# Performance work log

Hardware: AMD Instinct MI355X
Metric: run time of the kernel (lower is better)

Reference implementation:

```python
import jax, jax.numpy as jnp
import numpy as np

N = 16777216  # length of the returns series


def setup_inputs() -> dict:
    key = jax.random.key(0)
    returns = 0.01 * jax.random.normal(key, (N,), dtype=jnp.float32)
    return {
        "returns": returns,
        "omega": jnp.float32(0.01),
        "alpha": jnp.float32(0.1),
        "beta": jnp.float32(0.85),
    }


def reference(returns, omega, alpha, beta):
    # GARCH(1,1): h[0] = var(returns) (unbiased, matching torch.var default);
    # h[t] = omega + alpha * r[t-1]^2 + beta * h[t-1]
    h0 = jnp.var(returns, ddof=1)
    # drivers b_t = omega + alpha * r_{t-1}^2 for t = 1..n-1
    b = omega + alpha * jnp.square(returns[:-1])

    def step(h_prev, b_t):
        h_t = b_t + beta * h_prev
        return h_t, h_t

    _, h_rest = jax.lax.scan(step, h0, b)
    h = jnp.concatenate([h0[None], h_rest])  # [n]
    return jnp.sqrt(h), h
```

## Files before the change

kernel.cpp:

```cpp
#include <hip/hip_runtime.h>
#include <math.h>


#define KPW 2048
#define MAIN_BLOCK 256
#define FIX 256

typedef float v4f __attribute__((ext_vector_type(4)));

__global__ __launch_bounds__(MAIN_BLOCK, 8)
void garch_fused(const float* __restrict__ r, int n,
                 const float* __restrict__ pOmega, const float* __restrict__ pAlpha,
                 const float* __restrict__ pBeta,
                 float* __restrict__ out_sqrt, float* __restrict__ out_h,
                 double* __restrict__ partial) {
    const int lane = threadIdx.x & 63;
    const int wid  = threadIdx.x >> 6;
    const int gwave = (blockIdx.x * blockDim.x + threadIdx.x) >> 6;
    const int start = gwave * KPW;

    const float omega = *pOmega;
    const float alpha = *pAlpha;
    const float beta  = *pBeta;

    const float c1 = beta;
    const float c2 = c1 * c1;
    const float c4 = c2 * c2;
    const float c8 = c4 * c4;
    const float c16 = c8 * c8;
    const float c32 = c16 * c16;
    const float c64 = c32 * c32;
    const float c128 = c64 * c64;

    double acc_s = 0.0, acc_q = 0.0;

    if (start + KPW <= n) {
        float pw1 = 1.0f;
        { float p = c1; int e = lane;
          if (e & 1)  pw1 *= p; p *= p;
          if (e & 2)  pw1 *= p; p *= p;
          if (e & 4)  pw1 *= p; p *= p;
          if (e & 8)  pw1 *= p; p *= p;
          if (e & 16) pw1 *= p; p *= p;
          if (e & 32) pw1 *= p; }
        float pw32 = 1.0f;
        { float p = c32; int e = lane;
          if (e & 1)  pw32 *= p; p *= p;
          if (e & 2)  pw32 *= p; p *= p;
          if (e & 4)  pw32 *= p; p *= p;
          if (e & 8)  pw32 *= p; p *= p;
          if (e & 16) pw32 *= p; p *= p;
          if (e & 32) pw32 *= p; }

        const float4* r4p = (const float4*)r;
        const int base4 = (start >> 2) + lane * 8;

        float4 rv[8];
        #pragma unroll
        for (int k = 0; k < 8; ++k) rv[k] = r4p[base4 + k];

        float seed_ra = 0.0f, seed_rb = 0.0f, p0 = 0.0f;
        if (start > 0) {
            seed_ra = r[start - 2 - lane];
            seed_rb = r[start - 66 - lane];
            p0      = r[start - 1];
        }

        float h_prev = 0.0f;
        if (start > 0) {
            float ba = fmaf(alpha * seed_ra, seed_ra, omega);
            float bb = fmaf(alpha * seed_rb, seed_rb, omega);
            float part = pw1 * fmaf(c64, bb, ba);
            for (int d = 1; d < 64; d <<= 1) part += __shfl_xor(part, d, 64);
            h_prev = part;
        }

        #pragma unroll
        for (int k = 0; k < 8; k += 2) {
            float4 a = rv[k], b = rv[k + 1];
            float sf = ((a.x + a.y) + (a.z + a.w)) + ((b.x + b.y) + (b.z + b.w));
            float qf = fmaf(a.x, a.x, fmaf(a.y, a.y, fmaf(a.z, a.z, a.w * a.w)));
            qf = fmaf(b.x, b.x, fmaf(b.y, b.y, fmaf(b.z, b.z, fmaf(b.w, b.w, qf))));
            acc_s += (double)sf;
            acc_q += (double)qf;
        }

        float pprev = __shfl_up(rv[7].w, 1, 64);
        if (lane == 0) pprev = p0;

        float prev = pprev;
        float B = 0.0f;
        #pragma unroll
        for (int k = 0; k < 8; ++k) {
            float4 v = rv[k];
            float bb;
            bb = fmaf(alpha * prev, prev, omega);
            if (k == 0) { if (start == 0 && lane == 0) bb = 0.0f; B = bb; }
            else B = fmaf(c1, B, bb);
            prev = v.x;
            bb = fmaf(alpha * prev, prev, omega); B = fmaf(c1, B, bb); prev = v.y;
            bb = fmaf(alpha * prev, prev, omega); B = fmaf(c1, B, bb); prev = v.z;
            bb = fmaf(alpha * prev, prev, omega); B = fmaf(c1, B, bb); prev = v.w;
        }

        float t;
        t = __shfl_up(B, 1, 64); if (lane >= 1) B = fmaf(c32,  t, B);
        t = __shfl_up(B, 2, 64); if (lane >= 2) B = fmaf(c64,  t, B);
        t = __shfl_up(B, 4, 64); if (lane >= 4) B = fmaf(c128, t, B);

        float Bex = __shfl_up(B, 1, 64);
        if (lane == 0) Bex = 0.0f;
        float h = fmaf(pw32, h_prev, Bex);

        prev = pprev;
        #pragma unroll
        for (int k = 0; k < 8; ++k) {
            float4 v = rv[k];
            float bb;
            bb = fmaf(alpha * prev, prev, omega);
            if (k == 0 && start == 0 && lane == 0) bb = 0.0f;
            float h0v = fmaf(c1, h, bb);            prev = v.x;
            bb = fmaf(alpha * prev, prev, omega);
            float h1v = fmaf(c1, h0v, bb);          prev = v.y;
            bb = fmaf(alpha * prev, prev, omega);
            float h2v = fmaf(c1, h1v, bb);          prev = v.z;
            bb = fmaf(alpha * prev, prev, omega);
            float h3v = fmaf(c1, h2v, bb);          prev = v.w;
            h = h3v;

            v4f hs = {h0v, h1v, h2v, h3v};
            v4f sq = {sqrtf(h0v), sqrtf(h1v), sqrtf(h2v), sqrtf(h3v)};
            ((v4f*)out_h)[base4 + k]    = hs;
            ((v4f*)out_sqrt)[base4 + k] = sq;
        }
    } else if (start < n) {
        float h_prev = 0.0f;
        if (start > 0) {
            float pw1 = 1.0f;
            { float p = c1; int e = lane;
              if (e & 1)  pw1 *= p; p *= p;
              if (e & 2)  pw1 *= p; p *= p;
              if (e & 4)  pw1 *= p; p *= p;
              if (e & 8)  pw1 *= p; p *= p;
              if (e & 16) pw1 *= p; p *= p;
              if (e & 32) pw1 *= p; }
            float ra = r[start - 2 - lane];
            float rb = r[start - 66 - lane];
            float ba = fmaf(alpha * ra, ra, omega);
            float bb = fmaf(alpha * rb, rb, omega);
            float part = pw1 * fmaf(c64, bb, ba);
            for (int d = 1; d < 64; d <<= 1) part += __shfl_xor(part, d, 64);
            h_prev = part;
        }
        if (lane == 0) {
            float h = h_prev;
            float prevr = (start > 0) ? r[start - 1] : 0.0f;
            for (int tt = start; tt < n; ++tt) {
                float bb = fmaf(alpha * prevr, prevr, omega);
                if (tt == 0) bb = 0.0f;
                float hv = fmaf(beta, h, bb);
                out_sqrt[tt] = sqrtf(hv);
                out_h[tt] = hv;
                h = hv;
                prevr = r[tt];
                acc_s += (double)prevr;
                acc_q += (double)prevr * prevr;
            }
        }
    }

    for (int d = 1; d < 64; d <<= 1) {
        acc_s += __shfl_xor(acc_s, d, 64);
        acc_q += __shfl_xor(acc_q, d, 64);
    }
    __shared__ double ls[MAIN_BLOCK / 64], lq[MAIN_BLOCK / 64];
    if (lane == 0) { ls[wid] = acc_s; lq[wid] = acc_q; }
    __syncthreads();
    if (threadIdx.x == 0) {
        double S = 0.0, Q = 0.0;
        for (int w = 0; w < (int)(blockDim.x >> 6); ++w) { S += ls[w]; Q += lq[w]; }
        partial[2 * blockIdx.x]     = S;
        partial[2 * blockIdx.x + 1] = Q;
    }
}

__global__ void garch_finalize(const double* __restrict__ partial, int nblocks, int n,
                               const float* __restrict__ r,
                               const float* __restrict__ pOmega,
                               const float* __restrict__ pAlpha,
                               const float* __restrict__ pBeta,
                               float* __restrict__ out_sqrt, float* __restrict__ out_h) {
    __shared__ float rbuf[FIX];
    int fix = (n < FIX) ? n : FIX;
    for (int i = threadIdx.x; i < fix - 1; i += blockDim.x) rbuf[i] = r[i];

    double s = 0.0, q = 0.0;
    for (int i = threadIdx.x; i < nblocks; i += blockDim.x) {
        s += partial[2 * i];
        q += partial[2 * i + 1];
    }
    for (int d = 1; d < 64; d <<= 1) {
        s += __shfl_xor(s, d, 64);
        q += __shfl_xor(q, d, 64);
    }
    __shared__ double ls[4], lq[4];
    int wid = threadIdx.x >> 6, lane = threadIdx.x & 63;
    if (lane == 0) { ls[wid] = s; lq[wid] = q; }
    __syncthreads();
    if (threadIdx.x == 0) {
        double S = 0.0, Q = 0.0;
        for (int w = 0; w < (int)(blockDim.x >> 6); ++w) { S += ls[w]; Q += lq[w]; }
        double mean = S / (double)n;
        double var = (Q - (double)n * mean * mean) / (double)(n - 1);
        float h0 = (float)var;
        float omega = *pOmega, alpha = *pAlpha, beta = *pBeta;

        float h = h0;
        if (n > 0) { out_h[0] = h; out_sqrt[0] = sqrtf(h); }
        for (int t = 1; t < fix; ++t) {
            float rr = rbuf[t - 1];
            float b = fmaf(alpha * rr, rr, omega);
            h = fmaf(beta, h, b);
            out_h[t] = h;
            out_sqrt[t] = sqrtf(h);
        }
    }
}

extern "C" void kernel_launch(void* const* d_in, const int* in_sizes, int n_in,
                              void* d_out, int out_size, void* d_ws, size_t ws_size,
                              hipStream_t stream) {
    const float* r      = (const float*)d_in[0];
    const float* pOmega = (const float*)d_in[1];
    const float* pAlpha = (const float*)d_in[2];
    const float* pBeta  = (const float*)d_in[3];
    int n = in_sizes[0];

    float* out_sqrt = (float*)d_out;
    float* out_h    = out_sqrt + n;

    double* partial = (double*)d_ws;

    int elems_per_block = KPW * (MAIN_BLOCK / 64);
    int nblocks = (n + elems_per_block - 1) / elems_per_block;

    garch_fused<<<nblocks, MAIN_BLOCK, 0, stream>>>(
        r, n, pOmega, pAlpha, pBeta, out_sqrt, out_h, partial);
    garch_finalize<<<1, 256, 0, stream>>>(
        partial, nblocks, n, r, pOmega, pAlpha, pBeta, out_sqrt, out_h);
}
```

Before: 238.4 us.

## Switch wave scan to strided coalesced float4 layout with per-segment full-wave scans

Each lane now loads and stores float4 elements strided by 64 (fully coalesced per instruction) instead of 8 contiguous float4s per lane. The scan is restructured into 8 sequential segments, each doing a 6-step cross-lane shuffle scan with carry propagation via lane 63. This targets memory coalescing on loads and stores, at the cost of many more shuffles and a serial dependency chain across segments.

```diff
diff --git a/kernel.cpp b/kernel.cpp
--- a/kernel.cpp
+++ b/kernel.cpp
@@ -25,6 +25,7 @@
 
     const float c1 = beta;
     const float c2 = c1 * c1;
+    const float c3 = c2 * c1;
     const float c4 = c2 * c2;
     const float c8 = c4 * c4;
     const float c16 = c8 * c8;
@@ -43,33 +44,30 @@
           if (e & 8)  pw1 *= p; p *= p;
           if (e & 16) pw1 *= p; p *= p;
           if (e & 32) pw1 *= p; }
-        float pw32 = 1.0f;
-        { float p = c32; int e = lane;
-          if (e & 1)  pw32 *= p; p *= p;
-          if (e & 2)  pw32 *= p; p *= p;
-          if (e & 4)  pw32 *= p; p *= p;
-          if (e & 8)  pw32 *= p; p *= p;
-          if (e & 16) pw32 *= p; p *= p;
-          if (e & 32) pw32 *= p; }
+        float pw4 = 1.0f;
+        { float p = c4; int e = lane;
+          if (e & 1)  pw4 *= p; p *= p;
+          if (e & 2)  pw4 *= p; p *= p;
+          if (e & 4)  pw4 *= p; p *= p;
+          if (e & 8)  pw4 *= p; p *= p;
+          if (e & 16) pw4 *= p; p *= p;
+          if (e & 32) pw4 *= p; }
 
         const float4* r4p = (const float4*)r;
-        const int base4 = (start >> 2) + lane * 8;
+        const int b4 = (start >> 2) + lane;
 
         float4 rv[8];
         #pragma unroll
-        for (int k = 0; k < 8; ++k) rv[k] = r4p[base4 + k];
-
-        float seed_ra = 0.0f, seed_rb = 0.0f, p0 = 0.0f;
+        for (int k = 0; k < 8; ++k) rv[k] = r4p[b4 + 64 * k];
+
+        float h_prev = 0.0f;
+        float carry_r = 0.0f;
         if (start > 0) {
-            seed_ra = r[start - 2 - lane];
-            seed_rb = r[start - 66 - lane];
-            p0      = r[start - 1];
-        }
-
-        float h_prev = 0.0f;
-        if (start > 0) {
-            float ba = fmaf(alpha * seed_ra, seed_ra, omega);
-            float bb = fmaf(alpha * seed_rb, seed_rb, omega);
+            float ra = r[start - 2 - lane];
+            float rb = r[start - 66 - lane];
+            carry_r  = r[start - 1];
+            float ba = fmaf(alpha * ra, ra, omega);
+            float bb = fmaf(alpha * rb, rb, omega);
             float part = pw1 * fmaf(c64, bb, ba);
             for (int d = 1; d < 64; d <<= 1) part += __shfl_xor(part, d, 64);
             h_prev = part;
@@ -85,53 +83,47 @@
             acc_q += (double)qf;
         }
 
-        float pprev = __shfl_up(rv[7].w, 1, 64);
-        if (lane == 0) pprev = p0;
-
-        float prev = pprev;
-        float B = 0.0f;
         #pragma unroll
         for (int k = 0; k < 8; ++k) {
             float4 v = rv[k];
-            float bb;
-            bb = fmaf(alpha * prev, prev, omega);
-            if (k == 0) { if (start == 0 && lane == 0) bb = 0.0f; B = bb; }
-            else B = fmaf(c1, B, bb);
-            prev = v.x;
-            bb = fmaf(alpha * prev, prev, omega); B = fmaf(c1, B, bb); prev = v.y;
-            bb = fmaf(alpha * prev, prev, omega); B = fmaf(c1, B, bb); prev = v.z;
-            bb = fmaf(alpha * prev, prev, omega); B = fmaf(c1, B, bb); prev = v.w;
-        }
-
-        float t;
-        t = __shfl_up(B, 1, 64); if (lane >= 1) B = fmaf(c32,  t, B);
-        t = __shfl_up(B, 2, 64); if (lane >= 2) B = fmaf(c64,  t, B);
-        t = __shfl_up(B, 4, 64); if (lane >= 4) B = fmaf(c128, t, B);
-
-        float Bex = __shfl_up(B, 1, 64);
-        if (lane == 0) Bex = 0.0f;
-        float h = fmaf(pw32, h_prev, Bex);
-
-        prev = pprev;
-        #pragma unroll
-        for (int k = 0; k < 8; ++k) {
-            float4 v = rv[k];
-            float bb;
-            bb = fmaf(alpha * prev, prev, omega);
-            if (k == 0 && start == 0 && lane == 0) bb = 0.0f;
-            float h0v = fmaf(c1, h, bb);            prev = v.x;
-            bb = fmaf(alpha * prev, prev, omega);
-            float h1v = fmaf(c1, h0v, bb);          prev = v.y;
-            bb = fmaf(alpha * prev, prev, omega);
-            float h2v = fmaf(c1, h1v, bb);          prev = v.z;
-            bb = fmaf(alpha * prev, prev, omega);
-            float h3v = fmaf(c1, h2v, bb);          prev = v.w;
-            h = h3v;
+
+            float prevw = __shfl_up(v.w, 1, 64);
+            float segc  = (k == 0) ? carry_r : __shfl(rv[k - 1].w, 63, 64);
+            float prev  = (lane == 0) ? segc : prevw;
+
+            float b0 = fmaf(alpha * prev, prev, omega);
+            float b1 = fmaf(alpha * v.x, v.x, omega);
+            float b2 = fmaf(alpha * v.y, v.y, omega);
+            float b3 = fmaf(alpha * v.z, v.z, omega);
+            if (k == 0 && start == 0 && lane == 0) b0 = 0.0f;
+
+            float B = fmaf(c1, b2, b3);
+            B = fmaf(c2, b1, B);
+            B = fmaf(c3, b0, B);
+
+            float t;
+            t = __shfl_up(B, 1, 64);  if (lane >= 1)  B = fmaf(c4,   t, B);
+            t = __shfl_up(B, 2, 64);  if (lane >= 2)  B = fmaf(c8,   t, B);
+            t = __shfl_up(B, 4, 64);  if (lane >= 4)  B = fmaf(c16,  t, B);
+            t = __shfl_up(B, 8, 64);  if (lane >= 8)  B = fmaf(c32,  t, B);
+            t = __shfl_up(B, 16, 64); if (lane >= 16) B = fmaf(c64,  t, B);
+            t = __shfl_up(B, 32, 64); if (lane >= 32) B = fmaf(c128, t, B);
+
+            float Bex = __shfl_up(B, 1, 64);
+            if (lane == 0) Bex = 0.0f;
+            float hb = fmaf(pw4, h_prev, Bex);
+
+            float h0v = fmaf(c1, hb,  b0);
+            float h1v = fmaf(c1, h0v, b1);
+            float h2v = fmaf(c1, h1v, b2);
+            float h3v = fmaf(c1, h2v, b3);
 
             v4f hs = {h0v, h1v, h2v, h3v};
             v4f sq = {sqrtf(h0v), sqrtf(h1v), sqrtf(h2v), sqrtf(h3v)};
-            ((v4f*)out_h)[base4 + k]    = hs;
-            ((v4f*)out_sqrt)[base4 + k] = sq;
+            ((v4f*)out_h)[b4 + 64 * k]    = hs;
+            ((v4f*)out_sqrt)[b4 + 64 * k] = sq;
+
+            h_prev = __shfl(h3v, 63, 64);
         }
     } else if (start < n) {
         float h_prev = 0.0f;
```

Result: faster. 228.9 us (-4.0%).
